# Kernel tuning notes

Measured on AMD Instinct MI355X. Metric: run time of the kernel, lower is better.

## Reference

```python
import jax, jax.numpy as jnp
import numpy as np

B, Q, S, D, H = 8, 100, 4096, 256, 8
HD = D // H
EPS = 1e-5


def layer_norm(x, g, b):
    mu = jnp.mean(x, axis=-1, keepdims=True)
    var = jnp.mean(jnp.square(x - mu), axis=-1, keepdims=True)
    return (x - mu) * jax.lax.rsqrt(var + EPS) * g + b


def mha(q_in, k_in, v_in, w_in, b_in, w_out, b_out, bias=None):
    # torch nn.MultiheadAttention math (batch_first, dropout=0)
    wq, wk, wv = jnp.split(w_in, 3, axis=0)
    bq, bk, bv = jnp.split(b_in, 3, axis=0)
    Bq, Lq, _ = q_in.shape
    Lk = k_in.shape[1]
    q = (q_in @ wq.T + bq).reshape(Bq, Lq, H, HD)
    k = (k_in @ wk.T + bk).reshape(Bq, Lk, H, HD)
    v = (v_in @ wv.T + bv).reshape(Bq, Lk, H, HD)
    scores = jnp.einsum('bqhd,bkhd->bhqk', q, k) / jnp.sqrt(jnp.asarray(HD, q.dtype))
    if bias is not None:
        scores = scores + bias  # [B,1,Q,S] broadcast over heads (same per head)
    attn = jax.nn.softmax(scores, axis=-1)
    out = jnp.einsum('bhqk,bkhd->bqhd', attn, v).reshape(Bq, Lq, D)
    return out @ w_out.T + b_out


def setup_inputs() -> dict:
    key = jax.random.key(0)
    ks = jax.random.split(key, 12)
    s = 0.02
    return {
        'queries': jax.random.normal(ks[0], (B, Q, D), jnp.float32),
        'pixel_feat': jax.random.normal(ks[1], (B, S, D), jnp.float32),
        'prev_mask': jax.random.normal(ks[2], (B, Q, S), jnp.float32),
        'cross_in_w': jax.random.normal(ks[3], (3 * D, D), jnp.float32) * s,
        'cross_in_b': jnp.zeros((3 * D,), jnp.float32),
        'cross_out_w': jax.random.normal(ks[4], (D, D), jnp.float32) * s,
        'cross_out_b': jnp.zeros((D,), jnp.float32),
        'self_in_w': jax.random.normal(ks[5], (3 * D, D), jnp.float32) * s,
        'self_in_b': jnp.zeros((3 * D,), jnp.float32),
        'self_out_w': jax.random.normal(ks[6], (D, D), jnp.float32) * s,
        'self_out_b': jnp.zeros((D,), jnp.float32),
        'ln_cross_g': jnp.ones((D,), jnp.float32),
        'ln_cross_b': jnp.zeros((D,), jnp.float32),
        'ln_self_g': jnp.ones((D,), jnp.float32),
        'ln_self_b': jnp.zeros((D,), jnp.float32),
        'ln_ffn_g': jnp.ones((D,), jnp.float32),
        'ln_ffn_b': jnp.zeros((D,), jnp.float32),
        'ffn_w1': jax.random.normal(ks[7], (4 * D, D), jnp.float32) * s,
        'ffn_b1': jnp.zeros((4 * D,), jnp.float32),
        'ffn_w2': jax.random.normal(ks[8], (D, 4 * D), jnp.float32) * s,
        'ffn_b2': jnp.zeros((D,), jnp.float32),
    }


def reference(queries, pixel_feat, prev_mask,
              cross_in_w, cross_in_b, cross_out_w, cross_out_b,
              self_in_w, self_in_b, self_out_w, self_out_b,
              ln_cross_g, ln_cross_b, ln_self_g, ln_self_b, ln_ffn_g, ln_ffn_b,
              ffn_w1, ffn_b1, ffn_w2, ffn_b2):
    # masked cross-attn bias (no-grad region in torch; boolean ops have no grad)
    region = jax.nn.sigmoid(prev_mask) > 0.5                    # [B,Q,S]
    any_pos = jnp.any(region, axis=-1, keepdims=True)
    region = jnp.where(any_pos, region, jnp.ones_like(region))
    bias = (~region).astype(queries.dtype) * -10000.0
    bias = bias[:, None, :, :]                                  # [B,1,Q,S]

    q_out = mha(layer_norm(queries, ln_cross_g, ln_cross_b), pixel_feat, pixel_feat,
                cross_in_w, cross_in_b, cross_out_w, cross_out_b, bias)
    queries = queries + q_out

    q_norm = layer_norm(queries, ln_self_g, ln_self_b)
    q_out = mha(q_norm, q_norm, q_norm, self_in_w, self_in_b, self_out_w, self_out_b)
    queries = queries + q_out

    h = layer_norm(queries, ln_ffn_g, ln_ffn_b)
    h = jax.nn.gelu(h @ ffn_w1.T + ffn_b1, approximate=False) @ ffn_w2.T + ffn_b2
    return queries + h
```

## Files before the change

### kernel.cpp

```cpp
#include <hip/hip_runtime.h>
#include <hip/hip_bf16.h>
#include <math.h>

#define BQ 100
#define SB 8
#define SS 4096
#define DD 256
#define HH 8
#define HDD 32
#define NSPLIT 4
#define SCHUNK (SS / NSPLIT)
#define MROWS 800

typedef __attribute__((ext_vector_type(8))) short bf16x8;
typedef __attribute__((ext_vector_type(4))) float f32x4;

__device__ inline unsigned short f2bf(float f) {
    union { float f; unsigned u; } v; v.f = f;
    unsigned r = v.u + 0x7fff + ((v.u >> 16) & 1);
    return (unsigned short)(r >> 16);
}

__device__ inline unsigned pkbf(float x, float y) {
    union { __hip_bfloat162 h; unsigned u; } c;
    c.h = __float22bfloat162_rn(make_float2(x, y));
    return c.u;
}

__device__ inline bf16x8 load_bf8(const float* p) {
    float4 a = *(const float4*)p;
    float4 b = *(const float4*)(p + 4);
    union { unsigned u[4]; bf16x8 v; } r;
    r.u[0] = pkbf(a.x, a.y); r.u[1] = pkbf(a.z, a.w);
    r.u[2] = pkbf(b.x, b.y); r.u[3] = pkbf(b.z, b.w);
    return r.v;
}

typedef __attribute__((address_space(1))) const void gas_void;
typedef __attribute__((address_space(3))) void las_void;
__device__ inline void gl_lds16(const unsigned short* g, unsigned short* l) {
    __builtin_amdgcn_global_load_lds((gas_void*)g, (las_void*)l, 16, 0, 0);
}

#define TM 128
#define TN 128
#define QSCALE 0.17677669529663687f

#define WOFF_CW   0
#define WOFF_SIW  196608
#define WOFF_COW  393216
#define WOFF_SOW  458752
#define WOFF_F1   524288
#define WOFF_F2   786432
#define WTOT      1048576

__global__ __launch_bounds__(256) void wprep(
        const float* __restrict__ cw, const float* __restrict__ siw,
        const float* __restrict__ cow, const float* __restrict__ sow,
        const float* __restrict__ f1, const float* __restrict__ f2,
        const float* __restrict__ pix,
        unsigned short* __restrict__ o, unsigned short* __restrict__ abf) {
    int b = blockIdx.x;
    int t = threadIdx.x;
    if (b >= 512) {
        size_t off = (size_t)(b - 512) * 2048 + (size_t)t * 8;
        const float* p = pix + off;
        float4 a = *(const float4*)p;
        float4 c = *(const float4*)(p + 4);
        uint4 pk;
        pk.x = pkbf(a.x, a.y); pk.y = pkbf(a.z, a.w);
        pk.z = pkbf(c.x, c.y); pk.w = pkbf(c.z, c.w);
        *(uint4*)(abf + off) = pk;
        return;
    }
    const float* src; size_t so, doff;
    if (b < 96)       { src = cw;  so = (size_t)b * 2048;         doff = WOFF_CW; }
    else if (b < 192) { src = siw; so = (size_t)(b - 96) * 2048;  doff = WOFF_SIW; }
    else if (b < 224) { src = cow; so = (size_t)(b - 192) * 2048; doff = WOFF_COW; }
    else if (b < 256) { src = sow; so = (size_t)(b - 224) * 2048; doff = WOFF_SOW; }
    else if (b < 384) { src = f1;  so = (size_t)(b - 256) * 2048; doff = WOFF_F1; }
    else              { src = f2;  so = (size_t)(b - 384) * 2048; doff = WOFF_F2; }
    const float* p = src + so + (size_t)t * 8;
    float4 a = *(const float4*)p;
    float4 c = *(const float4*)(p + 4);
    uint4 pk;
    pk.x = pkbf(a.x, a.y); pk.y = pkbf(a.z, a.w);
    pk.z = pkbf(c.x, c.y); pk.w = pkbf(c.z, c.w);
    *(uint4*)(o + doff + so + (size_t)t * 8) = pk;
}

__global__ __launch_bounds__(256, 3) void stage1(
        const float* __restrict__ queries,
        const float* __restrict__ ln_g, const float* __restrict__ ln_b,
        const unsigned short* __restrict__ wbf,
        const float* __restrict__ cb,
        unsigned short* __restrict__ q_cross,
        const unsigned short* __restrict__ Abf,
        unsigned short* __restrict__ Kb, unsigned short* __restrict__ Vb,
        const float* __restrict__ mask, unsigned* __restrict__ Mbits) {
    __shared__ __align__(16) char smem[32768];
    const int bid = blockIdx.x;
    const int t = threadIdx.x;

    if (bid < 1024) {
        unsigned short* Sbuf = (unsigned short*)smem;
        const unsigned short* Wb = wbf + (size_t)DD * DD;
        const float* bias = cb + DD;
        int xcd = bid & 7, idx = bid >> 3;
        int mtile = xcd + 8 * (idx >> 2);
        int ntl = idx & 3;
        int m0 = mtile * TM, n0 = ntl * TN;
        int wave = t >> 6, lane = t & 63;
        int wm = (wave & 1) * 64, wn = (wave >> 1) * 64;
        int fr = lane & 15, quad = lane >> 4;
        f32x4 acc[4][4] = {};

        const int c0 = t, c1 = 256 + t;
        const int r0 = c0 >> 2, r1 = c1 >> 2;
        const int cc0 = (c0 & 3) ^ ((r0 >> 1) & 3);
        const int cc1 = (c1 & 3) ^ ((r1 >> 1) & 3);

        gl_lds16(Abf + (size_t)(m0 + r0) * DD + cc0 * 8, Sbuf + c0 * 8);
        gl_lds16(Abf + (size_t)(m0 + r1) * DD + cc1 * 8, Sbuf + c1 * 8);
        gl_lds16(Wb + (size_t)(n0 + r0) * DD + cc0 * 8, Sbuf + 4096 + c0 * 8);
        gl_lds16(Wb + (size_t)(n0 + r1) * DD + cc1 * 8, Sbuf + 4096 + c1 * 8);
        __syncthreads();

#pragma unroll
        for (int ks = 0; ks < 8; ks++) {
            unsigned short* Ab = Sbuf + (ks & 1) * 8192;
            unsigned short* Bb = Ab + 4096;
            if (ks < 7) {
                unsigned short* An = Sbuf + ((ks + 1) & 1) * 8192;
                unsigned short* Bn = An + 4096;
                int k0 = (ks + 1) * 32;
                gl_lds16(Abf + (size_t)(m0 + r0) * DD + k0 + cc0 * 8, An + c0 * 8);
                gl_lds16(Abf + (size_t)(m0 + r1) * DD + k0 + cc1 * 8, An + c1 * 8);
                gl_lds16(Wb + (size_t)(n0 + r0) * DD + k0 + cc0 * 8, Bn + c0 * 8);
                gl_lds16(Wb + (size_t)(n0 + r1) * DD + k0 + cc1 * 8, Bn + c1 * 8);
            }
            bf16x8 af[4], bv[4];
#pragma unroll
            for (int mi = 0; mi < 4; mi++) {
                int row = wm + mi * 16 + fr;
                int j = quad ^ ((row >> 1) & 3);
                af[mi] = *(const bf16x8*)(Ab + row * 32 + j * 8);
            }
#pragma unroll
            for (int ni = 0; ni < 4; ni++) {
                int row = wn + ni * 16 + fr;
                int j = quad ^ ((row >> 1) & 3);
                bv[ni] = *(const bf16x8*)(Bb + row * 32 + j * 8);
            }
#pragma unroll
            for (int mi = 0; mi < 4; mi++) {
                acc[mi][0] = __builtin_amdgcn_mfma_f32_16x16x32_bf16(af[mi], bv[0], acc[mi][0], 0, 0, 0);
                acc[mi][1] = __builtin_amdgcn_mfma_f32_16x16x32_bf16(af[mi], bv[1], acc[mi][1], 0, 0, 0);
                acc[mi][2] = __builtin_amdgcn_mfma_f32_16x16x32_bf16(af[mi], bv[2], acc[mi][2], 0, 0, 0);
                acc[mi][3] = __builtin_amdgcn_mfma_f32_16x16x32_bf16(af[mi], bv[3], acc[mi][3], 0, 0, 0);
            }
            __syncthreads();
        }
#pragma unroll
        for (int ni = 0; ni < 4; ni++) {
            int n = n0 + wn + ni * 16 + fr;
            float bv = bias[n];
            int hh = (n >> 5) & 7, d = n & 31;
            if (n < 256) {
#pragma unroll
                for (int mi = 0; mi < 4; mi++) {
#pragma unroll
                    for (int r = 0; r < 4; r++) {
                        int m = m0 + wm + mi * 16 + quad * 4 + r;
                        int bb = m >> 12, s = m & (SS - 1);
                        Kb[((((size_t)bb * HH + hh) * SS + s) << 5) + d] =
                            f2bf(acc[mi][ni][r] + bv);
                    }
                }
            } else {
#pragma unroll
                for (int mi = 0; mi < 4; mi++) {
                    int m = m0 + wm + mi * 16 + quad * 4;
                    int bb = m >> 12, s = m & (SS - 1);
                    union { unsigned short u[4]; uint2 v; } pk;
#pragma unroll
                    for (int r = 0; r < 4; r++)
                        pk.u[r] = f2bf(acc[mi][ni][r] + bv);
                    *(uint2*)&Vb[(((size_t)bb * HH + hh) * 32 + d) * SS + s] = pk.v;
                }
            }
        }
    } else if (bid < 1824) {
        int row = bid - 1024;
        unsigned* words = (unsigned*)smem;
        unsigned* orred = (unsigned*)(smem + 512);
        int w = t >> 6, lane = t & 63;
        const float* mp = mask + (size_t)row * SS + lane;
        float mv[16];
#pragma unroll
        for (int i = 0; i < 16; i++) mv[i] = mp[(w * 16 + i) * 64];
        unsigned lor = 0;
#pragma unroll
        for (int i = 0; i < 16; i++) {
            unsigned long long bal = __ballot(mv[i] > 0.f);
            if (lane == 0) {
                words[(w * 16 + i) * 2] = (unsigned)bal;
                words[(w * 16 + i) * 2 + 1] = (unsigned)(bal >> 32);
            }
            lor |= (unsigned)(bal | (bal >> 32));
        }
        if (lane == 0) orred[w] = lor;
        __syncthreads();
        unsigned anyv = orred[0] | orred[1] | orred[2] | orred[3];
        if (t < 128) Mbits[(size_t)row * 128 + t] = anyv ? words[t] : 0xFFFFFFFFu;
    } else {
        typedef unsigned short (*arow_t)[264];
        arow_t Aq = (arow_t)smem;
        float* mu_s = (float*)(smem + 16896);
        float* rs_s = mu_s + 32;
        float (*prt)[8][2] = (float(*)[8][2])(rs_s + 32);
        int idx = bid - 1824;
        int nq = idx & 1, my = idx >> 1;
        int m0 = my * 32;
        int row = t & 31, cs = t >> 5;
        const float* xp = queries + (size_t)(m0 + row) * DD + cs * 32;
        float s = 0.f, ss = 0.f;
#pragma unroll
        for (int c = 0; c < 32; c += 4) {
            float4 v = *(const float4*)(xp + c);
            s += v.x + v.y + v.z + v.w;
            ss += v.x * v.x + v.y * v.y + v.z * v.z + v.w * v.w;
        }
        prt[row][cs][0] = s; prt[row][cs][1] = ss;
        __syncthreads();
        if (t < 32) {
            float sum = 0.f, sq = 0.f;
#pragma unroll
            for (int k = 0; k < 8; k++) { sum += prt[t][k][0]; sq += prt[t][k][1]; }
            float mu = sum * (1.0f / DD);
            float var = sq * (1.0f / DD) - mu * mu;
            mu_s[t] = mu;
            rs_s[t] = rsqrtf(var + 1e-5f);
        }
        __syncthreads();
        {
            float mu = mu_s[row], r = rs_s[row];
            int col0 = cs * 32;
#pragma unroll
            for (int c = 0; c < 32; c += 8) {
                int col = col0 + c;
                float4 v0 = *(const float4*)(xp + c);
                float4 v1 = *(const float4*)(xp + c + 4);
                float4 g0 = *(const float4*)(ln_g + col);
                float4 g1 = *(const float4*)(ln_g + col + 4);
                float4 b0 = *(const float4*)(ln_b + col);
                float4 b1 = *(const float4*)(ln_b + col + 4);
                uint4 pk;
                pk.x = pkbf((v0.x - mu) * r * g0.x + b0.x, (v0.y - mu) * r * g0.y + b0.y);
                pk.y = pkbf((v0.z - mu) * r * g0.z + b0.z, (v0.w - mu) * r * g0.w + b0.w);
                pk.z = pkbf((v1.x - mu) * r * g1.x + b1.x, (v1.y - mu) * r * g1.y + b1.y);
                pk.w = pkbf((v1.z - mu) * r * g1.z + b1.z, (v1.w - mu) * r * g1.w + b1.w);
                *(uint4*)&Aq[row][col] = pk;
            }
        }
        __syncthreads();
        int w = t >> 6, lane = t & 63;
        int fr = lane & 15, quad = lane >> 4;
        int n0 = nq * 128 + w * 32;
        f32x4 acc[2][2] = {};
        const unsigned short* Wq0 = wbf + (size_t)(n0 + fr) * DD + quad * 8;
        const unsigned short* Wq1 = Wq0 + (size_t)16 * DD;
#pragma unroll
        for (int k0 = 0; k0 < DD; k0 += 32) {
            bf16x8 a0 = *(const bf16x8*)&Aq[fr][k0 + quad * 8];
            bf16x8 a1 = *(const bf16x8*)&Aq[16 + fr][k0 + quad * 8];
            bf16x8 w0 = *(const bf16x8*)(Wq0 + k0);
            bf16x8 w1 = *(const bf16x8*)(Wq1 + k0);
            acc[0][0] = __builtin_amdgcn_mfma_f32_16x16x32_bf16(a0, w0, acc[0][0], 0, 0, 0);
            acc[0][1] = __builtin_amdgcn_mfma_f32_16x16x32_bf16(a0, w1, acc[0][1], 0, 0, 0);
            acc[1][0] = __builtin_amdgcn_mfma_f32_16x16x32_bf16(a1, w0, acc[1][0], 0, 0, 0);
            acc[1][1] = __builtin_amdgcn_mfma_f32_16x16x32_bf16(a1, w1, acc[1][1], 0, 0, 0);
        }
#pragma unroll
        for (int ni = 0; ni < 2; ni++) {
            int n = n0 + ni * 16 + fr;
            float bv = cb[n];
#pragma unroll
            for (int mi = 0; mi < 2; mi++) {
#pragma unroll
                for (int r = 0; r < 4; r++) {
                    int m = m0 + mi * 16 + quad * 4 + r;
                    q_cross[(size_t)m * DD + n] =
                        f2bf((acc[mi][ni][r] + bv) * QSCALE);
                }
            }
        }
    }
}

template<int MODE>
__global__ __launch_bounds__(64, 4) void ln_gemm(
        const float* __restrict__ X, const float* __restrict__ gam,
        const float* __restrict__ bet,
        const unsigned short* __restrict__ W, const float* __restrict__ bias,
        const float* __restrict__ res,
        float* __restrict__ C, unsigned short* __restrict__ Cb, int N) {
    __shared__ unsigned short As[32][264];
    __shared__ float mu_s[32], rs_s[32];
    __shared__ float prt[32][2][2];
    const int t = threadIdx.x;
    const int fr = t & 15, quad = t >> 4;
    const int m0 = blockIdx.y * 32, n0 = blockIdx.x * 32;
    const int row = t & 31, half = t >> 5;

    const float* xp = X + (size_t)(m0 + row) * DD + half * 128;
    float s = 0.f, ss = 0.f;
#pragma unroll
    for (int c = 0; c < 128; c += 4) {
        float4 v = *(const float4*)(xp + c);
        s += v.x + v.y + v.z + v.w;
        ss += v.x * v.x + v.y * v.y + v.z * v.z + v.w * v.w;
    }
    prt[row][half][0] = s;
    prt[row][half][1] = ss;
    __syncthreads();
    if (t < 32) {
        float sum = prt[t][0][0] + prt[t][1][0];
        float sq  = prt[t][0][1] + prt[t][1][1];
        float mu = sum * (1.0f / DD);
        float var = sq * (1.0f / DD) - mu * mu;
        mu_s[t] = mu;
        rs_s[t] = rsqrtf(var + 1e-5f);
    }
    __syncthreads();
    {
        float mu = mu_s[row], r = rs_s[row];
#pragma unroll
        for (int c = 0; c < 128; c += 8) {
            int col = half * 128 + c;
            float4 v0 = *(const float4*)(xp + c);
            float4 v1 = *(const float4*)(xp + c + 4);
            float4 g0 = *(const float4*)(gam + col);
            float4 g1 = *(const float4*)(gam + col + 4);
            float4 b0 = *(const float4*)(bet + col);
            float4 b1 = *(const float4*)(bet + col + 4);
            uint4 pk;
            pk.x = pkbf((v0.x - mu) * r * g0.x + b0.x, (v0.y - mu) * r * g0.y + b0.y);
            pk.y = pkbf((v0.z - mu) * r * g0.z + b0.z, (v0.w - mu) * r * g0.w + b0.w);
            pk.z = pkbf((v1.x - mu) * r * g1.x + b1.x, (v1.y - mu) * r * g1.y + b1.y);
            pk.w = pkbf((v1.z - mu) * r * g1.z + b1.z, (v1.w - mu) * r * g1.w + b1.w);
            *(uint4*)&As[row][col] = pk;
        }
    }
    __syncthreads();

    f32x4 acc[2][2] = {};
    const unsigned short* Wp0 = W + (size_t)(n0 + fr) * DD + quad * 8;
    const unsigned short* Wp1 = Wp0 + (size_t)16 * DD;
#pragma unroll
    for (int k0 = 0; k0 < DD; k0 += 32) {
        bf16x8 a0 = *(const bf16x8*)&As[fr][k0 + quad * 8];
        bf16x8 a1 = *(const bf16x8*)&As[16 + fr][k0 + quad * 8];
        bf16x8 w0 = *(const bf16x8*)(Wp0 + k0);
        bf16x8 w1 = *(const bf16x8*)(Wp1 + k0);
        acc[0][0] = __builtin_amdgcn_mfma_f32_16x16x32_bf16(a0, w0, acc[0][0], 0, 0, 0);
        acc[0][1] = __builtin_amdgcn_mfma_f32_16x16x32_bf16(a0, w1, acc[0][1], 0, 0, 0);
        acc[1][0] = __builtin_amdgcn_mfma_f32_16x16x32_bf16(a1, w0, acc[1][0], 0, 0, 0);
        acc[1][1] = __builtin_amdgcn_mfma_f32_16x16x32_bf16(a1, w1, acc[1][1], 0, 0, 0);
    }

#pragma unroll
    for (int ni = 0; ni < 2; ni++) {
        int n = n0 + ni * 16 + fr;
        float bv = bias[n];
#pragma unroll
        for (int mi = 0; mi < 2; mi++) {
#pragma unroll
            for (int r = 0; r < 4; r++) {
                int m = m0 + mi * 16 + quad * 4 + r;
                float v = acc[mi][ni][r] + bv;
                if (MODE == 1) {
                    v = 0.5f * v * (1.0f + erff(v * 0.70710678118654752f));
                    Cb[(size_t)m * N + n] = f2bf(v);
                } else if (MODE == 2) {
                    v += res[(size_t)m * N + n];
                    C[(size_t)m * N + n] = v;
                } else if (MODE == 3) {
                    if (n < 256) v *= QSCALE;
                    Cb[(size_t)m * N + n] = f2bf(v);
                } else {
                    C[(size_t)m * N + n] = v;
                }
            }
        }
    }
}

__global__ __launch_bounds__(64, 4) void comb_gemm(
        const float* __restrict__ Opart, const float* __restrict__ mpart,
        const float* __restrict__ lpart,
        const unsigned short* __restrict__ W, const float* __restrict__ bias,
        const float* __restrict__ res,
        float* __restrict__ C) {
    __shared__ unsigned short As[32][264];
    const int t = threadIdx.x;
    const int fr = t & 15, quad = t >> 4;
    const int m0 = blockIdx.y * 32, n0 = blockIdx.x * 32;
    const int row = t & 31, half = t >> 5;

    {
        int m = m0 + row;
        int b = m / BQ, q = m % BQ;
#pragma unroll
        for (int h = half * 4; h < half * 4 + 4; h++) {
            float mv[NSPLIT], wsp[NSPLIT];
            float mstar = -1e30f;
#pragma unroll
            for (int sp = 0; sp < NSPLIT; sp++) {
                mv[sp] = mpart[((size_t)(b * NSPLIT + sp) * HH + h) * BQ + q];
                mstar = fmaxf(mstar, mv[sp]);
            }
            float lstar = 0.f;
#pragma unroll
            for (int sp = 0; sp < NSPLIT; sp++) {
                wsp[sp] = __expf(mv[sp] - mstar);
                lstar += lpart[((size_t)(b * NSPLIT + sp) * HH + h) * BQ + q] * wsp[sp];
            }
            float inv = 1.0f / lstar;
#pragma unroll
            for (int d = 0; d < HDD; d += 8) {
                float o[8] = {};
#pragma unroll
                for (int sp = 0; sp < NSPLIT; sp++) {
                    const float* op = Opart +
                        ((size_t)(b * NSPLIT + sp) * BQ + q) * DD + h * HDD + d;
                    float4 a = *(const float4*)op;
                    float4 b4 = *(const float4*)(op + 4);
                    o[0] += a.x * wsp[sp];  o[1] += a.y * wsp[sp];
                    o[2] += a.z * wsp[sp];  o[3] += a.w * wsp[sp];
                    o[4] += b4.x * wsp[sp]; o[5] += b4.y * wsp[sp];
                    o[6] += b4.z * wsp[sp]; o[7] += b4.w * wsp[sp];
                }
                uint4 pk;
                pk.x = pkbf(o[0] * inv, o[1] * inv);
                pk.y = pkbf(o[2] * inv, o[3] * inv);
                pk.z = pkbf(o[4] * inv, o[5] * inv);
                pk.w = pkbf(o[6] * inv, o[7] * inv);
                *(uint4*)&As[row][h * HDD + d] = pk;
            }
        }
    }
    __syncthreads();

    f32x4 acc[2][2] = {};
    const unsigned short* Wp0 = W + (size_t)(n0 + fr) * DD + quad * 8;
    const unsigned short* Wp1 = Wp0 + (size_t)16 * DD;
#pragma unroll
    for (int k0 = 0; k0 < DD; k0 += 32) {
        bf16x8 a0 = *(const bf16x8*)&As[fr][k0 + quad * 8];
        bf16x8 a1 = *(const bf16x8*)&As[16 + fr][k0 + quad * 8];
        bf16x8 w0 = *(const bf16x8*)(Wp0 + k0);
        bf16x8 w1 = *(const bf16x8*)(Wp1 + k0);
        acc[0][0] = __builtin_amdgcn_mfma_f32_16x16x32_bf16(a0, w0, acc[0][0], 0, 0, 0);
        acc[0][1] = __builtin_amdgcn_mfma_f32_16x16x32_bf16(a0, w1, acc[0][1], 0, 0, 0);
        acc[1][0] = __builtin_amdgcn_mfma_f32_16x16x32_bf16(a1, w0, acc[1][0], 0, 0, 0);
        acc[1][1] = __builtin_amdgcn_mfma_f32_16x16x32_bf16(a1, w1, acc[1][1], 0, 0, 0);
    }

#pragma unroll
    for (int ni = 0; ni < 2; ni++) {
        int n = n0 + ni * 16 + fr;
        float bv = bias[n];
#pragma unroll
        for (int mi = 0; mi < 2; mi++) {
#pragma unroll
            for (int r = 0; r < 4; r++) {
                int m = m0 + mi * 16 + quad * 4 + r;
                float v = acc[mi][ni][r] + bv + res[(size_t)m * DD + n];
                C[(size_t)m * DD + n] = v;
            }
        }
    }
}

template<int KK, int SPLITK, int MODE>
__global__ __launch_bounds__(64, 4) void gemm_skinny2(
        const unsigned short* __restrict__ A, const unsigned short* __restrict__ W,
        const float* __restrict__ bias, const float* __restrict__ res,
        float* __restrict__ C, float* __restrict__ Cp, int N) {
    const int lane = threadIdx.x;
    const int fr = lane & 15, quad = lane >> 4;
    const int m0 = blockIdx.y * 32;
    const int n0 = blockIdx.x * 32;
    const int sk = blockIdx.z;
    const int KCH = KK / SPLITK;

    f32x4 acc[2][2] = {};
    const unsigned short* Ap0 = A + (size_t)(m0 + fr) * KK + sk * KCH + quad * 8;
    const unsigned short* Ap1 = Ap0 + (size_t)16 * KK;
    const unsigned short* Wp0 = W + (size_t)(n0 + fr) * KK + sk * KCH + quad * 8;
    const unsigned short* Wp1 = Wp0 + (size_t)16 * KK;

#pragma unroll
    for (int k0 = 0; k0 < KCH; k0 += 32) {
        bf16x8 a0 = *(const bf16x8*)(Ap0 + k0);
        bf16x8 a1 = *(const bf16x8*)(Ap1 + k0);
        bf16x8 w0 = *(const bf16x8*)(Wp0 + k0);
        bf16x8 w1 = *(const bf16x8*)(Wp1 + k0);
        acc[0][0] = __builtin_amdgcn_mfma_f32_16x16x32_bf16(a0, w0, acc[0][0], 0, 0, 0);
        acc[0][1] = __builtin_amdgcn_mfma_f32_16x16x32_bf16(a0, w1, acc[0][1], 0, 0, 0);
        acc[1][0] = __builtin_amdgcn_mfma_f32_16x16x32_bf16(a1, w0, acc[1][0], 0, 0, 0);
        acc[1][1] = __builtin_amdgcn_mfma_f32_16x16x32_bf16(a1, w1, acc[1][1], 0, 0, 0);
    }

    if (SPLITK == 1) {
#pragma unroll
        for (int ni = 0; ni < 2; ni++) {
            int n = n0 + ni * 16 + fr;
            float bv = bias[n];
#pragma unroll
            for (int mi = 0; mi < 2; mi++) {
#pragma unroll
                for (int r = 0; r < 4; r++) {
                    int m = m0 + mi * 16 + quad * 4 + r;
                    float v = acc[mi][ni][r] + bv;
                    if (MODE == 1) {
                        v = 0.5f * v * (1.0f + erff(v * 0.70710678118654752f));
                    } else if (MODE == 2) {
                        v += res[(size_t)m * N + n];
                    }
                    C[(size_t)m * N + n] = v;
                }
            }
        }
    } else {
        float* dst = Cp + (size_t)sk * MROWS * N;
#pragma unroll
        for (int ni = 0; ni < 2; ni++) {
            int n = n0 + ni * 16 + fr;
#pragma unroll
            for (int mi = 0; mi < 2; mi++) {
#pragma unroll
                for (int r = 0; r < 4; r++) {
                    int m = m0 + mi * 16 + quad * 4 + r;
                    dst[(size_t)m * N + n] = acc[mi][ni][r];
                }
            }
        }
    }
}

template<int SPLITK, int MODE>
__global__ void gemm_combine(const float* __restrict__ Cp,
                             const float* __restrict__ bias,
                             const float* __restrict__ res,
                             float* __restrict__ C, int N) {
    int m = blockIdx.x;
    for (int n = threadIdx.x; n < N; n += 256) {
        float v = bias[n];
#pragma unroll
        for (int sk = 0; sk < SPLITK; sk++)
            v += Cp[((size_t)sk * MROWS + m) * N + n];
        if (MODE == 1) {
            v = 0.5f * v * (1.0f + erff(v * 0.70710678118654752f));
        } else if (MODE == 2) {
            v += res[(size_t)m * N + n];
        }
        C[(size_t)m * N + n] = v;
    }
}

#define QT 64
#define ST 128

__global__ __launch_bounds__(256) void cross_attn_mfma(
        const unsigned short* __restrict__ Qm,
        const unsigned short* __restrict__ Kb,
        const unsigned short* __restrict__ Vb,
        const unsigned* __restrict__ Mbits,
        float* __restrict__ Opart,
        float* __restrict__ mpart,
        float* __restrict__ lpart) {
    __shared__ unsigned short Qs[QT][40];
    __shared__ unsigned short Ks[ST][40];
    __shared__ unsigned short Vt[HDD][136];
    __shared__ unsigned short Ps[QT][136];
    __shared__ unsigned Mq[QT][4];
    __shared__ float4 redm[QT];
    __shared__ float4 reds[QT];
    __shared__ float m_s[QT], alpha_s[QT], l_s[QT];

    const int qb = blockIdx.x, h = blockIdx.y;
    const int b = blockIdx.z / NSPLIT, sp = blockIdx.z % NSPLIT;
    const int t = threadIdx.x;
    const int w = t >> 6, lane = t & 63;
    const int fr = lane & 15, quad = lane >> 4;
    const int q0 = qb * QT;
    const int qlim = min(BQ - q0, QT);

    {
        int q = t >> 2, c0 = (t & 3) * 8;
        uint4 pq = {0, 0, 0, 0};
        if (q < qlim)
            pq = *(const uint4*)(Qm + (size_t)(b * BQ + q0 + q) * DD + h * HDD + c0);
        *(uint4*)&Qs[q][c0] = pq;
        if (t < QT) { m_s[t] = -1e30f; l_s[t] = 0.f; }
    }

    f32x4 oacc[2] = {};
    const unsigned short* Kbase = Kb + (((size_t)(b * HH + h)) * SS << 5);
    const unsigned short* Vbase = Vb + (((size_t)(b * HH + h)) << 5) * SS;

    for (int s0 = sp * SCHUNK; s0 < (sp + 1) * SCHUNK; s0 += ST) {
        __syncthreads();
        {
            int r = t >> 1, half = t & 1;
            const unsigned short* kp = Kbase + ((size_t)(s0 + r) << 5) + half * 16;
            *(uint4*)&Ks[r][half * 16] = *(const uint4*)kp;
            *(uint4*)&Ks[r][half * 16 + 8] = *(const uint4*)(kp + 8);
            int d = t >> 3, c = (t & 7) * 16;
            const unsigned short* vp = Vbase + (size_t)d * SS + s0 + c;
            *(uint4*)&Vt[d][c] = *(const uint4*)vp;
            *(uint4*)&Vt[d][c + 8] = *(const uint4*)(vp + 8);
        }
        {
            int q = t >> 2, wd = t & 3;
            unsigned mword = 0xFFFFFFFFu;
            if (q < qlim)
                mword = Mbits[(size_t)(b * BQ + q0 + q) * 128 + (s0 >> 5) + wd];
            Mq[q][wd] = mword;
        }
        __syncthreads();

        bf16x8 af[2];
#pragma unroll
        for (int mt = 0; mt < 2; mt++)
            af[mt] = *(const bf16x8*)&Ks[w * 32 + mt * 16 + fr][quad * 8];
        f32x4 st[2][4];
#pragma unroll
        for (int nt = 0; nt < 4; nt++) {
            bf16x8 bq = *(const bf16x8*)&Qs[nt * 16 + fr][quad * 8];
#pragma unroll
            for (int mt = 0; mt < 2; mt++) {
                f32x4 z = {0.f, 0.f, 0.f, 0.f};
                st[mt][nt] = __builtin_amdgcn_mfma_f32_16x16x32_bf16(af[mt], bq, z, 0, 0, 0);
            }
        }

        float mo[4];
#pragma unroll
        for (int nt = 0; nt < 4; nt++) mo[nt] = m_s[nt * 16 + fr];

        float pmax[4];
#pragma unroll
        for (int nt = 0; nt < 4; nt++) {
            unsigned mword = Mq[nt * 16 + fr][w];
            pmax[nt] = -1e30f;
#pragma unroll
            for (int mt = 0; mt < 2; mt++)
#pragma unroll
                for (int r = 0; r < 4; r++) {
                    int bitpos = mt * 16 + quad * 4 + r;
                    float v = st[mt][nt][r];
                    if (!((mword >> bitpos) & 1u)) v -= 10000.f;
                    st[mt][nt][r] = v;
                    pmax[nt] = fmaxf(pmax[nt], v);
                }
        }
#pragma unroll
        for (int nt = 0; nt < 4; nt++) {
            pmax[nt] = fmaxf(pmax[nt], __shfl_xor(pmax[nt], 16));
            pmax[nt] = fmaxf(pmax[nt], __shfl_xor(pmax[nt], 32));
        }
        if (quad == 0) {
#pragma unroll
            for (int nt = 0; nt < 4; nt++)
                ((float*)&redm[nt * 16 + fr])[w] = pmax[nt];
        }
        __syncthreads();

        float mn[4], al[4];
#pragma unroll
        for (int nt = 0; nt < 4; nt++) {
            float4 rr = redm[nt * 16 + fr];
            float mt4 = fmaxf(fmaxf(rr.x, rr.y), fmaxf(rr.z, rr.w));
            mn[nt] = fmaxf(mo[nt], mt4);
            al[nt] = __expf(mo[nt] - mn[nt]);
        }
        if (w == 0 && quad == 0) {
#pragma unroll
            for (int nt = 0; nt < 4; nt++) {
                m_s[nt * 16 + fr] = mn[nt];
                alpha_s[nt * 16 + fr] = al[nt];
            }
        }

        float psum[4];
#pragma unroll
        for (int nt = 0; nt < 4; nt++) {
            psum[nt] = 0.f;
#pragma unroll
            for (int mt = 0; mt < 2; mt++) {
                float p0 = __expf(st[mt][nt][0] - mn[nt]);
                float p1 = __expf(st[mt][nt][1] - mn[nt]);
                float p2 = __expf(st[mt][nt][2] - mn[nt]);
                float p3 = __expf(st[mt][nt][3] - mn[nt]);
                psum[nt] += p0 + p1 + p2 + p3;
                uint2 pk;
                pk.x = pkbf(p0, p1);
                pk.y = pkbf(p2, p3);
                *(uint2*)&Ps[nt * 16 + fr][w * 32 + mt * 16 + quad * 4] = pk;
            }
        }
#pragma unroll
        for (int nt = 0; nt < 4; nt++) {
            psum[nt] += __shfl_xor(psum[nt], 16);
            psum[nt] += __shfl_xor(psum[nt], 32);
        }
        if (quad == 0) {
#pragma unroll
            for (int nt = 0; nt < 4; nt++)
                ((float*)&reds[nt * 16 + fr])[w] = psum[nt];
        }
        __syncthreads();

        if (w == 0 && quad == 0) {
#pragma unroll
            for (int nt = 0; nt < 4; nt++) {
                int q = nt * 16 + fr;
                float4 ssum = reds[q];
                l_s[q] = l_s[q] * al[nt] + (ssum.x + ssum.y + ssum.z + ssum.w);
            }
        }

#pragma unroll
        for (int r = 0; r < 4; r++) {
            float a = alpha_s[w * 16 + quad * 4 + r];
            oacc[0][r] *= a; oacc[1][r] *= a;
        }
#pragma unroll
        for (int k0 = 0; k0 < ST; k0 += 32) {
            bf16x8 ap = *(const bf16x8*)&Ps[w * 16 + fr][k0 + quad * 8];
            bf16x8 bv0 = *(const bf16x8*)&Vt[fr][k0 + quad * 8];
            bf16x8 bv1 = *(const bf16x8*)&Vt[16 + fr][k0 + quad * 8];
            oacc[0] = __builtin_amdgcn_mfma_f32_16x16x32_bf16(ap, bv0, oacc[0], 0, 0, 0);
            oacc[1] = __builtin_amdgcn_mfma_f32_16x16x32_bf16(ap, bv1, oacc[1], 0, 0, 0);
        }
    }
    __syncthreads();

    int part = b * NSPLIT + sp;
    if (t < qlim) {
        mpart[((size_t)part * HH + h) * BQ + q0 + t] = m_s[t];
        lpart[((size_t)part * HH + h) * BQ + q0 + t] = l_s[t];
    }
#pragma unroll
    for (int nd = 0; nd < 2; nd++) {
#pragma unroll
        for (int r = 0; r < 4; r++) {
            int q = w * 16 + quad * 4 + r;
            if (q < qlim)
                Opart[((size_t)part * BQ + q0 + q) * DD + h * HDD + nd * 16 + fr] = oacc[nd][r];
        }
    }
}

__global__ __launch_bounds__(256) void self_attn_mfma(
        const unsigned short* __restrict__ qkv, unsigned short* __restrict__ Out) {
    __shared__ unsigned short Qs[128][40];
    __shared__ unsigned short Vt[HDD][136];
    __shared__ unsigned short Ps[112][136];
    __shared__ float red[112][17];
    __shared__ float m_s[112], l_s[112];

    const int h = blockIdx.x, b = blockIdx.y;
    const int t = threadIdx.x;
    const int w = t >> 6, lane = t & 63;
    const int fr = lane & 15, quad = lane >> 4;

    {
        int r = t >> 1, half = t & 1;
        uint4 z = {0, 0, 0, 0};
        uint4 p0 = z, p1 = z, v0 = z, v1 = z;
        if (r < BQ) {
            const unsigned short* qp = qkv + (size_t)(b * BQ + r) * 768 + h * HDD + half * 16;
            p0 = *(const uint4*)qp;
            p1 = *(const uint4*)(qp + 8);
            const unsigned short* vp = qp + 512;
            v0 = *(const uint4*)vp;
            v1 = *(const uint4*)(vp + 8);
        }
        *(uint4*)&Qs[r][half * 16] = p0;
        *(uint4*)&Qs[r][half * 16 + 8] = p1;
        union { uint4 u; unsigned short s[8]; } a, c;
        a.u = v0; c.u = v1;
#pragma unroll
        for (int j = 0; j < 8; j++) Vt[half * 16 + j][r] = a.s[j];
#pragma unroll
        for (int j = 0; j < 8; j++) Vt[half * 16 + 8 + j][r] = c.s[j];
    }
    __syncthreads();

    bf16x8 af[2];
#pragma unroll
    for (int mt = 0; mt < 2; mt++) {
        int s = w * 32 + mt * 16 + fr;
        bf16x8 kz = {0, 0, 0, 0, 0, 0, 0, 0};
        af[mt] = kz;
        if (s < BQ)
            af[mt] = *(const bf16x8*)(qkv + (size_t)(b * BQ + s) * 768 + 256 + h * HDD + quad * 8);
    }
    f32x4 st[2][7];
#pragma unroll
    for (int nt = 0; nt < 7; nt++) {
        bf16x8 bq = *(const bf16x8*)&Qs[nt * 16 + fr][quad * 8];
#pragma unroll
        for (int mt = 0; mt < 2; mt++) {
            f32x4 z = {0.f, 0.f, 0.f, 0.f};
            st[mt][nt] = __builtin_amdgcn_mfma_f32_16x16x32_bf16(af[mt], bq, z, 0, 0, 0);
        }
    }

    float pmax[7];
#pragma unroll
    for (int nt = 0; nt < 7; nt++) {
        pmax[nt] = -1e30f;
#pragma unroll
        for (int mt = 0; mt < 2; mt++)
#pragma unroll
            for (int r = 0; r < 4; r++) {
                int s = w * 32 + mt * 16 + quad * 4 + r;
                float v = st[mt][nt][r];
                if (s >= BQ) v = -1e30f;
                st[mt][nt][r] = v;
                pmax[nt] = fmaxf(pmax[nt], v);
            }
        red[nt * 16 + fr][w * 4 + quad] = pmax[nt];
    }
    __syncthreads();
    if (t < 112) {
        float m = -1e30f;
#pragma unroll
        for (int k = 0; k < 16; k++) m = fmaxf(m, red[t][k]);
        m_s[t] = m;
    }
    __syncthreads();

    float psum[7];
#pragma unroll
    for (int nt = 0; nt < 7; nt++) {
        float mrow = m_s[nt * 16 + fr];
        psum[nt] = 0.f;
#pragma unroll
        for (int mt = 0; mt < 2; mt++) {
            float p0 = __expf(st[mt][nt][0] - mrow);
            float p1 = __expf(st[mt][nt][1] - mrow);
            float p2 = __expf(st[mt][nt][2] - mrow);
            float p3 = __expf(st[mt][nt][3] - mrow);
            psum[nt] += p0 + p1 + p2 + p3;
            uint2 pk;
            pk.x = pkbf(p0, p1);
            pk.y = pkbf(p2, p3);
            *(uint2*)&Ps[nt * 16 + fr][w * 32 + mt * 16 + quad * 4] = pk;
        }
        red[nt * 16 + fr][w * 4 + quad] = psum[nt];
    }
    __syncthreads();
    if (t < 112) {
        float s = 0.f;
#pragma unroll
        for (int k = 0; k < 16; k++) s += red[t][k];
        l_s[t] = s;
    }
    __syncthreads();

    f32x4 oacc[2][2] = {};
#pragma unroll
    for (int ti = 0; ti < 2; ti++) {
        int qt = w + ti * 4;
        if (qt < 7) {
#pragma unroll
            for (int k0 = 0; k0 < 128; k0 += 32) {
                bf16x8 ap = *(const bf16x8*)&Ps[qt * 16 + fr][k0 + quad * 8];
                bf16x8 bv0 = *(const bf16x8*)&Vt[fr][k0 + quad * 8];
                bf16x8 bv1 = *(const bf16x8*)&Vt[16 + fr][k0 + quad * 8];
                oacc[ti][0] = __builtin_amdgcn_mfma_f32_16x16x32_bf16(ap, bv0, oacc[ti][0], 0, 0, 0);
                oacc[ti][1] = __builtin_amdgcn_mfma_f32_16x16x32_bf16(ap, bv1, oacc[ti][1], 0, 0, 0);
            }
        }
    }
#pragma unroll
    for (int ti = 0; ti < 2; ti++) {
        int qt = w + ti * 4;
        if (qt < 7) {
#pragma unroll
            for (int nd = 0; nd < 2; nd++) {
#pragma unroll
                for (int r = 0; r < 4; r++) {
                    int q = qt * 16 + quad * 4 + r;
                    if (q < BQ) {
                        float inv = 1.0f / l_s[q];
                        Out[(size_t)(b * BQ + q) * DD + h * HDD + nd * 16 + fr] =
                            f2bf(oacc[ti][nd][r] * inv);
                    }
                }
            }
        }
    }
}

extern "C" void kernel_launch(void* const* d_in, const int* in_sizes, int n_in,
                              void* d_out, int out_size, void* d_ws, size_t ws_size,
                              hipStream_t stream) {
    const float* queries    = (const float*)d_in[0];
    const float* pixel_feat = (const float*)d_in[1];
    const float* prev_mask  = (const float*)d_in[2];
    const float* cross_in_w  = (const float*)d_in[3];
    const float* cross_in_b  = (const float*)d_in[4];
    const float* cross_out_w = (const float*)d_in[5];
    const float* cross_out_b = (const float*)d_in[6];
    const float* self_in_w   = (const float*)d_in[7];
    const float* self_in_b   = (const float*)d_in[8];
    const float* self_out_w  = (const float*)d_in[9];
    const float* self_out_b  = (const float*)d_in[10];
    const float* ln_cross_g  = (const float*)d_in[11];
    const float* ln_cross_b  = (const float*)d_in[12];
    const float* ln_self_g   = (const float*)d_in[13];
    const float* ln_self_b   = (const float*)d_in[14];
    const float* ln_ffn_g    = (const float*)d_in[15];
    const float* ln_ffn_b    = (const float*)d_in[16];
    const float* ffn_w1 = (const float*)d_in[17];
    const float* ffn_b1 = (const float*)d_in[18];
    const float* ffn_w2 = (const float*)d_in[19];
    const float* ffn_b2 = (const float*)d_in[20];
    float* out = (float*)d_out;

    const int NQ = SB * BQ;
    const int NK = SB * SS;

    float* ws = (float*)d_ws;
    unsigned* Mbits = (unsigned*)ws;   ws += (size_t)NQ * 128;
    unsigned short* q_crossb = (unsigned short*)ws;  ws += (size_t)NQ * DD;
    unsigned short* Kbk = (unsigned short*)ws;
    ws += (size_t)NK * DD / 2;
    unsigned short* Vbk = (unsigned short*)ws;
    ws += (size_t)NK * DD / 2;
    float* queries1 = ws;              ws += (size_t)NQ * DD;
    unsigned short* qkvb = (unsigned short*)ws;      ws += (size_t)NQ * 3 * DD;
    unsigned short* attn2b = (unsigned short*)ws;    ws += (size_t)NQ * DD;
    float* queries2 = ws;              ws += (size_t)NQ * DD;
    unsigned short* Hbf = (unsigned short*)ws;       ws += (size_t)NQ * 4 * DD;
    float* Csplit   = ws;              ws += (size_t)4 * MROWS * DD;
    float* Opart    = ws;              ws += (size_t)SB * NSPLIT * BQ * DD;
    float* mpart    = ws;              ws += (size_t)SB * NSPLIT * HH * BQ;
    float* lpart    = ws;              ws += (size_t)SB * NSPLIT * HH * BQ;
    unsigned short* wbf = (unsigned short*)ws;
    ws += WTOT / 2;
    unsigned short* Abf = (unsigned short*)ws;

    wprep<<<4608, 256, 0, stream>>>(
        cross_in_w, self_in_w, cross_out_w, self_out_w, ffn_w1, ffn_w2,
        pixel_feat, wbf, Abf);

    stage1<<<1874, 256, 0, stream>>>(
        queries, ln_cross_g, ln_cross_b, wbf, cross_in_b, q_crossb,
        Abf, Kbk, Vbk, prev_mask, Mbits);

    cross_attn_mfma<<<dim3(2, HH, SB * NSPLIT), 256, 0, stream>>>(
        q_crossb, Kbk, Vbk, Mbits, Opart, mpart, lpart);
    comb_gemm<<<dim3(8, 25), 64, 0, stream>>>(
        Opart, mpart, lpart, wbf + WOFF_COW, cross_out_b, queries, queries1);

    ln_gemm<3><<<dim3(24, 25), 64, 0, stream>>>(
        queries1, ln_self_g, ln_self_b, wbf + WOFF_SIW, self_in_b, nullptr,
        nullptr, qkvb, 3 * DD);
    self_attn_mfma<<<dim3(HH, SB), 256, 0, stream>>>(qkvb, attn2b);
    gemm_skinny2<256, 1, 2><<<dim3(8, 25), 64, 0, stream>>>(
        attn2b, wbf + WOFF_SOW, self_out_b, queries1, queries2, nullptr, DD);

    ln_gemm<1><<<dim3(32, 25), 64, 0, stream>>>(
        queries2, ln_ffn_g, ln_ffn_b, wbf + WOFF_F1, ffn_b1, nullptr,
        nullptr, Hbf, 4 * DD);
    gemm_skinny2<1024, 4, 2><<<dim3(8, 25, 4), 64, 0, stream>>>(
        Hbf, wbf + WOFF_F2, ffn_b2, nullptr, nullptr, Csplit, DD);
    gemm_combine<4, 2><<<MROWS, 256, 0, stream>>>(
        Csplit, ffn_b2, queries2, out, DD);
}
```

Measured before the change: 226.6 us.

## Load K and mask directly to registers and prefetch V tiles in cross-attention

The cross-attention kernel no longer stages K and the mask bits through shared memory. Each wave now loads its own MFMA K fragments and mask words straight from global memory. V for the next tile is prefetched into registers while the current tile is processed, and one of the two barriers per iteration is removed. This cuts LDS traffic and synchronisation and hides global latency, at the cost of extra registers and less coalesced per-lane K loads.

```diff
diff --git a/kernel.cpp b/kernel.cpp
--- a/kernel.cpp
+++ b/kernel.cpp
@@ -25,15 +25,6 @@
     union { __hip_bfloat162 h; unsigned u; } c;
     c.h = __float22bfloat162_rn(make_float2(x, y));
     return c.u;
-}
-
-__device__ inline bf16x8 load_bf8(const float* p) {
-    float4 a = *(const float4*)p;
-    float4 b = *(const float4*)(p + 4);
-    union { unsigned u[4]; bf16x8 v; } r;
-    r.u[0] = pkbf(a.x, a.y); r.u[1] = pkbf(a.z, a.w);
-    r.u[2] = pkbf(b.x, b.y); r.u[3] = pkbf(b.z, b.w);
-    return r.v;
 }
 
 typedef __attribute__((address_space(1))) const void gas_void;
@@ -582,10 +573,8 @@
         float* __restrict__ mpart,
         float* __restrict__ lpart) {
     __shared__ unsigned short Qs[QT][40];
-    __shared__ unsigned short Ks[ST][40];
     __shared__ unsigned short Vt[HDD][136];
     __shared__ unsigned short Ps[QT][136];
-    __shared__ unsigned Mq[QT][4];
     __shared__ float4 redm[QT];
     __shared__ float4 reds[QT];
     __shared__ float m_s[QT], alpha_s[QT], l_s[QT];
@@ -610,32 +599,39 @@
     f32x4 oacc[2] = {};
     const unsigned short* Kbase = Kb + (((size_t)(b * HH + h)) * SS << 5);
     const unsigned short* Vbase = Vb + (((size_t)(b * HH + h)) << 5) * SS;
-
-    for (int s0 = sp * SCHUNK; s0 < (sp + 1) * SCHUNK; s0 += ST) {
+    const int vd = t >> 3, vc = (t & 7) * 16;
+    const unsigned short* vrow = Vbase + (size_t)vd * SS;
+
+    const int send = (sp + 1) * SCHUNK;
+    uint4 vr0 = *(const uint4*)(vrow + sp * SCHUNK + vc);
+    uint4 vr1 = *(const uint4*)(vrow + sp * SCHUNK + vc + 8);
+
+    for (int s0 = sp * SCHUNK; s0 < send; s0 += ST) {
+        bf16x8 af[2];
+#pragma unroll
+        for (int mt = 0; mt < 2; mt++)
+            af[mt] = *(const bf16x8*)(Kbase +
+                ((size_t)(s0 + w * 32 + mt * 16 + fr) << 5) + quad * 8);
+        unsigned mw[4];
+#pragma unroll
+        for (int nt = 0; nt < 4; nt++) {
+            int q = nt * 16 + fr;
+            mw[nt] = (q < qlim)
+                ? Mbits[(size_t)(b * BQ + q0 + q) * 128 + (s0 >> 5) + w]
+                : 0xFFFFFFFFu;
+        }
         __syncthreads();
-        {
-            int r = t >> 1, half = t & 1;
-            const unsigned short* kp = Kbase + ((size_t)(s0 + r) << 5) + half * 16;
-            *(uint4*)&Ks[r][half * 16] = *(const uint4*)kp;
-            *(uint4*)&Ks[r][half * 16 + 8] = *(const uint4*)(kp + 8);
-            int d = t >> 3, c = (t & 7) * 16;
-            const unsigned short* vp = Vbase + (size_t)d * SS + s0 + c;
-            *(uint4*)&Vt[d][c] = *(const uint4*)vp;
-            *(uint4*)&Vt[d][c + 8] = *(const uint4*)(vp + 8);
-        }
-        {
-            int q = t >> 2, wd = t & 3;
-            unsigned mword = 0xFFFFFFFFu;
-            if (q < qlim)
-                mword = Mbits[(size_t)(b * BQ + q0 + q) * 128 + (s0 >> 5) + wd];
-            Mq[q][wd] = mword;
-        }
-        __syncthreads();
-
-        bf16x8 af[2];
-#pragma unroll
-        for (int mt = 0; mt < 2; mt++)
-            af[mt] = *(const bf16x8*)&Ks[w * 32 + mt * 16 + fr][quad * 8];
+        *(uint4*)&Vt[vd][vc] = vr0;
+        *(uint4*)&Vt[vd][vc + 8] = vr1;
+        if (s0 + ST < send) {
+            vr0 = *(const uint4*)(vrow + s0 + ST + vc);
+            vr1 = *(const uint4*)(vrow + s0 + ST + vc + 8);
+        }
+
+        float mo[4];
+#pragma unroll
+        for (int nt = 0; nt < 4; nt++) mo[nt] = m_s[nt * 16 + fr];
+
         f32x4 st[2][4];
 #pragma unroll
         for (int nt = 0; nt < 4; nt++) {
@@ -647,14 +643,9 @@
             }
         }
 
-        float mo[4];
-#pragma unroll
-        for (int nt = 0; nt < 4; nt++) mo[nt] = m_s[nt * 16 + fr];
-
         float pmax[4];
 #pragma unroll
         for (int nt = 0; nt < 4; nt++) {
-            unsigned mword = Mq[nt * 16 + fr][w];
             pmax[nt] = -1e30f;
 #pragma unroll
             for (int mt = 0; mt < 2; mt++)
@@ -662,7 +653,7 @@
                 for (int r = 0; r < 4; r++) {
                     int bitpos = mt * 16 + quad * 4 + r;
                     float v = st[mt][nt][r];
-                    if (!((mword >> bitpos) & 1u)) v -= 10000.f;
+                    if (!((mw[nt] >> bitpos) & 1u)) v -= 10000.f;
                     st[mt][nt][r] = v;
                     pmax[nt] = fmaxf(pmax[nt], v);
                 }
```

Measured after the change: 228.7 us. About the same (+0.9%).
